# Optimization experiments

Hardware: AMD Instinct MI355X
Metric: run time of the kernel (lower is better)

## Reference

```python
import jax, jax.numpy as jnp
import numpy as np

BN_EPS = 1e-5
TAU = 1.0  # gumbel temperature

def setup_inputs() -> dict:
    key = jax.random.key(0)
    ks = jax.random.split(key, 6)
    B, O, F, H, HID = 32, 4096, 256, 8, 128
    x = jax.random.normal(ks[0], (B, O, F), dtype=jnp.float32)
    gumbel_noise = jax.random.gumbel(ks[1], (B, O, H), dtype=jnp.float32)
    W_in = jax.random.normal(ks[2], (F, HID), dtype=jnp.float32) * (1.0 / np.sqrt(F))
    b_in = jnp.zeros((HID,), jnp.float32)
    W_blk = jax.random.normal(ks[3], (HID, HID), dtype=jnp.float32) * (1.0 / np.sqrt(HID))
    b_blk = jnp.zeros((HID,), jnp.float32)
    bn_gamma = jnp.ones((HID,), jnp.float32)
    bn_beta = jnp.zeros((HID,), jnp.float32)
    W_fc = jax.random.normal(ks[4], (HID, H), dtype=jnp.float32) * (1.0 / np.sqrt(HID))
    b_fc = jnp.zeros((H,), jnp.float32)
    return {"x": x, "gumbel_noise": gumbel_noise, "W_in": W_in, "b_in": b_in,
            "W_blk": W_blk, "b_blk": b_blk, "bn_gamma": bn_gamma, "bn_beta": bn_beta,
            "W_fc": W_fc, "b_fc": b_fc}

def reference(x, gumbel_noise, W_in, b_in, W_blk, b_blk, bn_gamma, bn_beta, W_fc, b_fc):
    B, O, F = x.shape
    xf = x.reshape(B * O, F)
    # DynamicNetwork head: input linear + relu, one residual block (Linear+BN+ReLU), fc
    h = jax.nn.relu(xf @ W_in + b_in)  # (B*O, HID)
    z = h @ W_blk + b_blk
    mu = z.mean(axis=0)
    var = z.var(axis=0)  # biased var, matches BatchNorm training normalization
    z = (z - mu) * jax.lax.rsqrt(var + BN_EPS) * bn_gamma + bn_beta
    h = jax.nn.relu(z) + h  # residual
    logits = (h @ W_fc + b_fc).reshape(B, O, -1)  # (B, O, H)
    # mask out zero-norm observations
    mask = (jnp.linalg.norm(x, axis=2) != 0)[..., None].astype(x.dtype)  # (B, O, 1)
    logits = logits * mask
    # gumbel softmax over observation dim (soft)
    w = jax.nn.softmax((logits + gumbel_noise) / TAU, axis=1)  # (B, O, H)
    # weighted sum pooling: algebraically the repeat-multiply-sum in the original
    pooled = jnp.einsum('boh,bof->bhf', w, x)  # (B, H, F)
    return pooled.reshape(B, -1)  # (B, H*F)
```

## Files before the change

### kernel.cpp

```cpp
#include <hip/hip_runtime.h>
#include <math.h>

#define MB_ 131072
#define F_  256
#define HID_ 128
#define H_  8
#define O_  4096
#define B_  32

typedef __attribute__((ext_vector_type(8))) short short8;
typedef __attribute__((ext_vector_type(4))) float f32x4;

static __device__ __forceinline__ unsigned short f2bf(float f) {
    unsigned int u = __float_as_uint(f);
    unsigned int r = (u + 0x7fffu + ((u >> 16) & 1u)) >> 16;
    return (unsigned short)r;
}
static __device__ __forceinline__ float bflo(unsigned int u) {
    return __uint_as_float(u << 16);
}
static __device__ __forceinline__ float bfhi(unsigned int u) {
    return __uint_as_float(u & 0xffff0000u);
}
static __device__ __forceinline__ unsigned int fkey(float f) {
    unsigned int u = __float_as_uint(f);
    return (u & 0x80000000u) ? ~u : (u | 0x80000000u);
}
static __device__ __forceinline__ short8 pack_bf16x8(const float4 a, const float4 b) {
    short8 r;
    r[0] = (short)f2bf(a.x); r[1] = (short)f2bf(a.y);
    r[2] = (short)f2bf(a.z); r[3] = (short)f2bf(a.w);
    r[4] = (short)f2bf(b.x); r[5] = (short)f2bf(b.y);
    r[6] = (short)f2bf(b.z); r[7] = (short)f2bf(b.w);
    return r;
}
static __device__ __forceinline__ void sync_lds() {
    asm volatile("s_waitcnt lgkmcnt(0)" ::: "memory");
    __builtin_amdgcn_s_barrier();
    __builtin_amdgcn_sched_barrier(0);
}

__global__ __launch_bounds__(256) void k_prep(
    const float* __restrict__ W_in, const float* __restrict__ W_blk,
    unsigned short* __restrict__ WinT, unsigned short* __restrict__ WblkT,
    unsigned int* __restrict__ Mmax)
{
    const int idx = blockIdx.x * 256 + threadIdx.x;
    if (idx < 256) Mmax[idx] = 0u;
    if (idx < 32768) {
        const int n = idx >> 8, k = idx & 255;
        WinT[idx] = f2bf(W_in[(size_t)k * HID_ + n]);
    } else {
        const int i2 = idx - 32768;
        const int n = i2 >> 7, k = i2 & 127;
        WblkT[i2] = f2bf(W_blk[(size_t)k * HID_ + n]);
    }
}

__global__ __launch_bounds__(512, 4) void k_fused(
    const float* __restrict__ x, const unsigned short* __restrict__ WinT,
    const float* __restrict__ b_in,
    const unsigned short* __restrict__ WblkT, const float* __restrict__ b_blk,
    unsigned short* __restrict__ h_out, unsigned short* __restrict__ z_out,
    float* __restrict__ mask_out,
    float* __restrict__ sumP, float* __restrict__ sumsqP)
{
    __shared__ unsigned short smem[16384];
    unsigned short* stg = smem;
    unsigned short* h_s = smem;

    const int tid = threadIdx.x;
    const int R0 = blockIdx.x * 128;
    const int wave = tid >> 6;
    const int wrow = wave >> 2;
    const int wcol = wave & 3;
    const int lane = tid & 63;
    const int lm = lane & 15, quad = lane >> 4;

    const int srow = tid >> 2, sch = tid & 3;
    const int sgo = srow * 32 + ((sch ^ ((srow >> 1) & 3)) << 3);
    const float* xb = x + (size_t)(R0 + srow) * F_ + sch * 8;

    int aoff[4];
#pragma unroll
    for (int mi = 0; mi < 4; mi++) {
        const int ar = wrow * 64 + mi * 16 + lm;
        aoff[mi] = ar * 32 + ((quad ^ ((ar >> 1) & 3)) << 3);
    }
    const unsigned short* wr0 = WinT + (size_t)(wcol * 32 + lm) * F_ + quad * 8;
    const unsigned short* wr1 = wr0 + (size_t)16 * F_;

    f32x4 acc[4][2];
#pragma unroll
    for (int i = 0; i < 4; i++)
#pragma unroll
        for (int j = 0; j < 2; j++) acc[i][j] = (f32x4){0.f, 0.f, 0.f, 0.f};
    float msq = 0.f;

    float4 c0 = *(const float4*)(xb);
    float4 c1 = *(const float4*)(xb + 4);

#pragma unroll
    for (int kt = 0; kt < 8; kt++) {
        float4 n0, n1;
        if (kt < 7) {
            n0 = *(const float4*)(xb + (kt + 1) * 32);
            n1 = *(const float4*)(xb + (kt + 1) * 32 + 4);
        }
        short8 bC[2];
        bC[0] = *(const short8*)(wr0 + kt * 32);
        bC[1] = *(const short8*)(wr1 + kt * 32);
        msq += c0.x * c0.x + c0.y * c0.y + c0.z * c0.z + c0.w * c0.w
             + c1.x * c1.x + c1.y * c1.y + c1.z * c1.z + c1.w * c1.w;
        *(short8*)(stg + (kt & 1) * 4096 + sgo) = pack_bf16x8(c0, c1);
        sync_lds();
        short8 af[4];
#pragma unroll
        for (int mi = 0; mi < 4; mi++)
            af[mi] = *(const short8*)(stg + (kt & 1) * 4096 + aoff[mi]);
#pragma unroll
        for (int mi = 0; mi < 4; mi++)
#pragma unroll
            for (int ni = 0; ni < 2; ni++)
                acc[mi][ni] = __builtin_amdgcn_mfma_f32_16x16x32_bf16(af[mi], bC[ni], acc[mi][ni], 0, 0, 0);
        if (kt < 7) { c0 = n0; c1 = n1; }
    }

    msq += __shfl_xor(msq, 1, 64);
    msq += __shfl_xor(msq, 2, 64);
    if ((tid & 3) == 0) mask_out[R0 + srow] = (msq != 0.f) ? 1.f : 0.f;

    __syncthreads();

    {
        float bcol[2];
#pragma unroll
        for (int ni = 0; ni < 2; ni++) bcol[ni] = b_in[wcol * 32 + ni * 16 + lm];
#pragma unroll
        for (int mi = 0; mi < 4; mi++)
#pragma unroll
            for (int r = 0; r < 4; r++) {
                const int rl = wrow * 64 + mi * 16 + quad * 4 + r;
#pragma unroll
                for (int ni = 0; ni < 2; ni++) {
                    const int col = wcol * 32 + ni * 16 + lm;
                    const float v = fmaxf(acc[mi][ni][r] + bcol[ni], 0.f);
                    h_s[rl * 128 + ((((col >> 3) ^ (rl & 7)) << 3) | (col & 7))] = f2bf(v);
                }
            }
    }
#pragma unroll
    for (int i = 0; i < 4; i++)
#pragma unroll
        for (int j = 0; j < 2; j++) acc[i][j] = (f32x4){0.f, 0.f, 0.f, 0.f};
    __syncthreads();

    {
        const int crow = tid >> 2, cb = tid & 3;
#pragma unroll
        for (int j = 0; j < 4; j++) {
            const int ch = cb * 4 + j;
            const short8 v = *(const short8*)(h_s + crow * 128 + ((ch ^ (crow & 7)) << 3));
            *(short8*)(h_out + (size_t)(R0 + crow) * HID_ + ch * 8) = v;
        }
    }

    {
        const unsigned short* wb0 = WblkT + (size_t)(wcol * 32 + lm) * HID_ + quad * 8;
        const unsigned short* wb1 = wb0 + (size_t)16 * HID_;
#pragma unroll
        for (int kt2 = 0; kt2 < 4; kt2++) {
            short8 wbf[2];
            wbf[0] = *(const short8*)(wb0 + kt2 * 32);
            wbf[1] = *(const short8*)(wb1 + kt2 * 32);
            short8 haf[4];
#pragma unroll
            for (int mi = 0; mi < 4; mi++) {
                const int hr = wrow * 64 + mi * 16 + lm;
                haf[mi] = *(const short8*)(h_s + hr * 128 + (((kt2 * 4 + quad) ^ (hr & 7)) << 3));
            }
#pragma unroll
            for (int mi = 0; mi < 4; mi++)
#pragma unroll
                for (int ni = 0; ni < 2; ni++)
                    acc[mi][ni] = __builtin_amdgcn_mfma_f32_16x16x32_bf16(haf[mi], wbf[ni], acc[mi][ni], 0, 0, 0);
        }
    }

    __syncthreads();

    {
        float bcol2[2];
#pragma unroll
        for (int ni = 0; ni < 2; ni++) bcol2[ni] = b_blk[wcol * 32 + ni * 16 + lm];
        float s_c[2] = {0.f, 0.f}, ss_c[2] = {0.f, 0.f};
#pragma unroll
        for (int mi = 0; mi < 4; mi++)
#pragma unroll
            for (int r = 0; r < 4; r++) {
                const int rl = wrow * 64 + mi * 16 + quad * 4 + r;
#pragma unroll
                for (int ni = 0; ni < 2; ni++) {
                    const int col = wcol * 32 + ni * 16 + lm;
                    const float zv = acc[mi][ni][r] + bcol2[ni];
                    s_c[ni] += zv;
                    ss_c[ni] += zv * zv;
                    h_s[rl * 128 + ((((col >> 3) ^ (rl & 7)) << 3) | (col & 7))] = f2bf(zv);
                }
            }
#pragma unroll
        for (int ni = 0; ni < 2; ni++) {
            s_c[ni]  += __shfl_xor(s_c[ni], 16, 64);
            s_c[ni]  += __shfl_xor(s_c[ni], 32, 64);
            ss_c[ni] += __shfl_xor(ss_c[ni], 16, 64);
            ss_c[ni] += __shfl_xor(ss_c[ni], 32, 64);
        }
        if (quad == 0) {
#pragma unroll
            for (int ni = 0; ni < 2; ni++) {
                const int col = wcol * 32 + ni * 16 + lm;
                sumP[((size_t)blockIdx.x * 2 + wrow) * 128 + col]   = s_c[ni];
                sumsqP[((size_t)blockIdx.x * 2 + wrow) * 128 + col] = ss_c[ni];
            }
        }
    }
    __syncthreads();

    {
        const int crow = tid >> 2, cb = tid & 3;
#pragma unroll
        for (int j = 0; j < 4; j++) {
            const int ch = cb * 4 + j;
            const short8 v = *(const short8*)(h_s + crow * 128 + ((ch ^ (crow & 7)) << 3));
            *(short8*)(z_out + (size_t)(R0 + crow) * HID_ + ch * 8) = v;
        }
    }
}

__global__ __launch_bounds__(256) void k_bnfin(
    const float* __restrict__ sumP, const float* __restrict__ sumsqP,
    const float* __restrict__ gamma, const float* __restrict__ beta,
    float* __restrict__ scale, float* __restrict__ shift)
{
    const int c = blockIdx.x;
    const int tid = threadIdx.x;
    float s = 0.f, ss = 0.f;
    for (int i = tid; i < 2048; i += 256) {
        s  += sumP[(size_t)i * 128 + c];
        ss += sumsqP[(size_t)i * 128 + c];
    }
#pragma unroll
    for (int off = 32; off; off >>= 1) {
        s  += __shfl_xor(s, off, 64);
        ss += __shfl_xor(ss, off, 64);
    }
    __shared__ float rs[4], rss[4];
    const int wid = tid >> 6, lane = tid & 63;
    if (lane == 0) { rs[wid] = s; rss[wid] = ss; }
    __syncthreads();
    if (tid == 0) {
        const float S  = rs[0] + rs[1] + rs[2] + rs[3];
        const float SS = rss[0] + rss[1] + rss[2] + rss[3];
        const float inv_m = 1.0f / (float)MB_;
        const float mu = S * inv_m;
        const float var = SS * inv_m - mu * mu;
        const float sc = gamma[c] * rsqrtf(var + 1e-5f);
        scale[c] = sc;
        shift[c] = beta[c] - mu * sc;
    }
}

__global__ __launch_bounds__(256) void k_logits(
    const unsigned short* __restrict__ h_in, const unsigned short* __restrict__ z_in,
    const float* __restrict__ scale, const float* __restrict__ shift,
    const float* __restrict__ W_fc, const float* __restrict__ b_fc,
    const float* __restrict__ mask, const float* __restrict__ gumbel,
    float* __restrict__ t_out, unsigned int* __restrict__ Mmax)
{
    __shared__ float wfc_s[1024];
    __shared__ float sc_s[128], sh_s[128];
    const int tid = threadIdx.x;
    for (int i = tid; i < 1024; i += 256) wfc_s[i] = W_fc[i];
    if (tid < 128) { sc_s[tid] = scale[tid]; sh_s[tid] = shift[tid]; }
    __syncthreads();

    const size_t row0 = (size_t)blockIdx.x * 512 + tid;
    const size_t row1 = row0 + 256;
    float a0[8], a1[8];
#pragma unroll
    for (int j = 0; j < 8; j++) { a0[j] = 0.f; a1[j] = 0.f; }

    const uint4* hp0 = (const uint4*)(h_in + row0 * HID_);
    const uint4* zq0 = (const uint4*)(z_in + row0 * HID_);
    const uint4* hp1 = (const uint4*)(h_in + row1 * HID_);
    const uint4* zq1 = (const uint4*)(z_in + row1 * HID_);

#pragma unroll 2
    for (int kc = 0; kc < 16; kc++) {
        const uint4 h0 = hp0[kc], z0 = zq0[kc];
        const uint4 h1 = hp1[kc], z1 = zq1[kc];
        const unsigned int hs0[4] = {h0.x, h0.y, h0.z, h0.w};
        const unsigned int zs0[4] = {z0.x, z0.y, z0.z, z0.w};
        const unsigned int hs1[4] = {h1.x, h1.y, h1.z, h1.w};
        const unsigned int zs1[4] = {z1.x, z1.y, z1.z, z1.w};
#pragma unroll
        for (int p = 0; p < 4; p++) {
            const int k = kc * 8 + p * 2;
            const float sck0 = sc_s[k], shk0 = sh_s[k];
            const float sck1 = sc_s[k + 1], shk1 = sh_s[k + 1];
            const float4 wA = *(const float4*)&wfc_s[k * 8];
            const float4 wB = *(const float4*)&wfc_s[k * 8 + 4];
            const float4 wC = *(const float4*)&wfc_s[k * 8 + 8];
            const float4 wD = *(const float4*)&wfc_s[k * 8 + 12];
            {
                const float hf0 = bflo(hs0[p]), hf1 = bfhi(hs0[p]);
                const float zf0 = bflo(zs0[p]), zf1 = bfhi(zs0[p]);
                const float hb0 = fmaxf(zf0 * sck0 + shk0, 0.f) + hf0;
                const float hb1 = fmaxf(zf1 * sck1 + shk1, 0.f) + hf1;
                a0[0] += hb0 * wA.x + hb1 * wC.x;  a0[1] += hb0 * wA.y + hb1 * wC.y;
                a0[2] += hb0 * wA.z + hb1 * wC.z;  a0[3] += hb0 * wA.w + hb1 * wC.w;
                a0[4] += hb0 * wB.x + hb1 * wD.x;  a0[5] += hb0 * wB.y + hb1 * wD.y;
                a0[6] += hb0 * wB.z + hb1 * wD.z;  a0[7] += hb0 * wB.w + hb1 * wD.w;
            }
            {
                const float hf0 = bflo(hs1[p]), hf1 = bfhi(hs1[p]);
                const float zf0 = bflo(zs1[p]), zf1 = bfhi(zs1[p]);
                const float hb0 = fmaxf(zf0 * sck0 + shk0, 0.f) + hf0;
                const float hb1 = fmaxf(zf1 * sck1 + shk1, 0.f) + hf1;
                a1[0] += hb0 * wA.x + hb1 * wC.x;  a1[1] += hb0 * wA.y + hb1 * wC.y;
                a1[2] += hb0 * wA.z + hb1 * wC.z;  a1[3] += hb0 * wA.w + hb1 * wC.w;
                a1[4] += hb0 * wB.x + hb1 * wD.x;  a1[5] += hb0 * wB.y + hb1 * wD.y;
                a1[6] += hb0 * wB.z + hb1 * wD.z;  a1[7] += hb0 * wB.w + hb1 * wD.w;
            }
        }
    }

    float bf[8];
#pragma unroll
    for (int j = 0; j < 8; j++) bf[j] = b_fc[j];
    const float mk0 = mask[row0], mk1 = mask[row1];
    float g0[8], g1[8];
    *(float4*)&g0[0] = *(const float4*)(gumbel + row0 * 8);
    *(float4*)&g0[4] = *(const float4*)(gumbel + row0 * 8 + 4);
    *(float4*)&g1[0] = *(const float4*)(gumbel + row1 * 8);
    *(float4*)&g1[4] = *(const float4*)(gumbel + row1 * 8 + 4);
    float t0[8], t1[8];
#pragma unroll
    for (int j = 0; j < 8; j++) {
        t0[j] = (a0[j] + bf[j]) * mk0 + g0[j];
        t1[j] = (a1[j] + bf[j]) * mk1 + g1[j];
    }
    *(float4*)(t_out + row0 * 8)     = *(float4*)&t0[0];
    *(float4*)(t_out + row0 * 8 + 4) = *(float4*)&t0[4];
    *(float4*)(t_out + row1 * 8)     = *(float4*)&t1[0];
    *(float4*)(t_out + row1 * 8 + 4) = *(float4*)&t1[4];

    float tm[8];
#pragma unroll
    for (int j = 0; j < 8; j++) tm[j] = fmaxf(t0[j], t1[j]);
#pragma unroll
    for (int off = 32; off; off >>= 1)
#pragma unroll
        for (int j = 0; j < 8; j++) tm[j] = fmaxf(tm[j], __shfl_xor(tm[j], off, 64));
    if ((tid & 63) == 0) {
        const int bb = blockIdx.x >> 3;
#pragma unroll
        for (int j = 0; j < 8; j++) atomicMax(&Mmax[bb * 8 + j], fkey(tm[j]));
    }
}

__global__ __launch_bounds__(256) void k_pool(
    const float* __restrict__ x, const float* __restrict__ t_in,
    const unsigned int* __restrict__ Mmax,
    float* __restrict__ pp, float* __restrict__ zp)
{
    __shared__ float ws_s[8][64];
    __shared__ float M_s[8];
    const int tid = threadIdx.x;
    const int oc = blockIdx.x;
    const int b  = blockIdx.y;
    if (tid < 8) {
        const unsigned int k = Mmax[b * 8 + tid];
        const unsigned int s = (k & 0x80000000u) ? (k & 0x7fffffffu) : ~k;
        M_s[tid] = __uint_as_float(s);
    }
    __syncthreads();
#pragma unroll
    for (int i = tid; i < 512; i += 256) {
        const int ol = i >> 3, hh = i & 7;
        const float tv = t_in[((size_t)b * O_ + oc * 64 + ol) * H_ + hh];
        ws_s[hh][ol] = __expf(tv - M_s[hh]);
    }
    __syncthreads();
    if (tid < 8) {
        float s = 0.f;
        for (int o = 0; o < 64; o++) s += ws_s[tid][o];
        zp[((size_t)oc * 32 + b) * 8 + tid] = s;
    }
    float acc[8];
#pragma unroll
    for (int hh = 0; hh < 8; hh++) acc[hh] = 0.f;
    const float* xp = x + ((size_t)b * O_ + oc * 64) * F_ + tid;
#pragma unroll 4
    for (int o = 0; o < 64; o++) {
        const float xv = xp[(size_t)o * F_];
#pragma unroll
        for (int hh = 0; hh < 8; hh++) acc[hh] += ws_s[hh][o] * xv;
    }
    float* outp = pp + ((size_t)oc * 32 + b) * 2048;
#pragma unroll
    for (int hh = 0; hh < 8; hh++) outp[hh * 256 + tid] = acc[hh];
}

__global__ __launch_bounds__(256) void k_reduce(
    const float* __restrict__ pp, const float* __restrict__ zp,
    float* __restrict__ out)
{
    const int blk = blockIdx.x;
    const int b = blk >> 3, hh = blk & 7;
    const int tid = threadIdx.x;
    __shared__ float invZ_s;
    if (tid < 64) {
        float z = zp[((size_t)tid * 32 + b) * 8 + hh];
#pragma unroll
        for (int off = 32; off; off >>= 1) z += __shfl_xor(z, off, 64);
        if (tid == 0) invZ_s = 1.f / z;
    }
    __syncthreads();
    float s = 0.f;
    const float* p0 = pp + (size_t)b * 2048 + hh * 256 + tid;
#pragma unroll 8
    for (int ocq = 0; ocq < 64; ocq++) s += p0[(size_t)ocq * 65536];
    out[(size_t)b * 2048 + hh * 256 + tid] = s * invZ_s;
}

extern "C" void kernel_launch(void* const* d_in, const int* in_sizes, int n_in,
                              void* d_out, int out_size, void* d_ws, size_t ws_size,
                              hipStream_t stream)
{
    const float* x      = (const float*)d_in[0];
    const float* gumbel = (const float*)d_in[1];
    const float* W_in   = (const float*)d_in[2];
    const float* b_in   = (const float*)d_in[3];
    const float* W_blk  = (const float*)d_in[4];
    const float* b_blk  = (const float*)d_in[5];
    const float* gamma  = (const float*)d_in[6];
    const float* beta   = (const float*)d_in[7];
    const float* W_fc   = (const float*)d_in[8];
    const float* b_fc   = (const float*)d_in[9];
    float* out = (float*)d_out;
    char* ws = (char*)d_ws;

    unsigned short* h_bf  = (unsigned short*)(ws + 0);
    float* pp     = (float*)(ws + 0);
    float* zp     = (float*)(ws + 16777216);
    unsigned short* z_bf  = (unsigned short*)(ws + 33554432);
    float* mask   = (float*)(ws + 67108864);
    float* sumP   = (float*)(ws + 67633152);
    float* sumsqP = (float*)(ws + 68681728);
    float* scale  = (float*)(ws + 69730304);
    float* shift  = (float*)(ws + 69730816);
    float* t_buf  = (float*)(ws + 69731328);
    unsigned int* Mmax = (unsigned int*)(ws + 73925632);
    unsigned short* WinT  = (unsigned short*)(ws + 73926656);
    unsigned short* WblkT = (unsigned short*)(ws + 73992192);

    k_prep<<<192, 256, 0, stream>>>(W_in, W_blk, WinT, WblkT, Mmax);
    k_fused<<<1024, 512, 0, stream>>>(x, WinT, b_in, WblkT, b_blk, h_bf, z_bf, mask, sumP, sumsqP);
    k_bnfin<<<128, 256, 0, stream>>>(sumP, sumsqP, gamma, beta, scale, shift);
    k_logits<<<256, 256, 0, stream>>>(h_bf, z_bf, scale, shift, W_fc, b_fc, mask, gumbel, t_buf, Mmax);
    k_pool<<<dim3(64, 32), 256, 0, stream>>>(x, t_buf, Mmax, pp, zp);
    k_reduce<<<256, 256, 0, stream>>>(pp, zp, out);
}
```

Measured before the change: 303.9 us.

## Stage x tiles via global_load_lds and convert to bf16 after the LDS read

Replaces the register-staged x loads (global load, pack to bf16, LDS store) with direct global-to-LDS DMA loads of fp32 data into a double-buffered, XOR-swizzled LDS tile. Each wave then reads fp32 from LDS, computes the row squared-norm for the mask, and packs to bf16 before the MFMA. The aim is to cut VGPR pressure and VALU/store work on the load path and overlap the prefetch with compute. In exchange, LDS traffic doubles because fp32 is stored, the bf16 conversion is repeated by all four wcol waves, and each k-step now waits on vmcnt(0) plus a barrier.

Result: slower. 311.0 us (+2.4%).

```diff
diff --git a/kernel.cpp b/kernel.cpp
--- a/kernel.cpp
+++ b/kernel.cpp
@@ -34,10 +34,10 @@
     r[6] = (short)f2bf(b.z); r[7] = (short)f2bf(b.w);
     return r;
 }
-static __device__ __forceinline__ void sync_lds() {
-    asm volatile("s_waitcnt lgkmcnt(0)" ::: "memory");
-    __builtin_amdgcn_s_barrier();
-    __builtin_amdgcn_sched_barrier(0);
+static __device__ __forceinline__ void gll16(const float* g, float* l) {
+    __builtin_amdgcn_global_load_lds(
+        (const __attribute__((address_space(1))) float*)g,
+        (__attribute__((address_space(3))) float*)l, 16, 0, 0);
 }
 
 __global__ __launch_bounds__(256) void k_prep(
@@ -66,7 +66,7 @@
     float* __restrict__ sumP, float* __restrict__ sumsqP)
 {
     __shared__ unsigned short smem[16384];
-    unsigned short* stg = smem;
+    float* stgf = (float*)smem;
     unsigned short* h_s = smem;
 
     const int tid = threadIdx.x;
@@ -77,15 +77,20 @@
     const int lane = tid & 63;
     const int lm = lane & 15, quad = lane >> 4;
 
-    const int srow = tid >> 2, sch = tid & 3;
-    const int sgo = srow * 32 + ((sch ^ ((srow >> 1) & 3)) << 3);
-    const float* xb = x + (size_t)(R0 + srow) * F_ + sch * 8;
-
-    int aoff[4];
+    const int r0s = wave * 16 + (lane >> 3);
+    const int r1s = r0s + 8;
+    const int cl0 = (lane & 7) ^ (r0s & 7);
+    const int cl1 = (lane & 7) ^ (r1s & 7);
+    const float* g0 = x + (size_t)(R0 + r0s) * F_ + cl0 * 4;
+    const float* g1 = x + (size_t)(R0 + r1s) * F_ + cl1 * 4;
+    const int lbase = wave * 512;
+
+    int aoff[4][2];
 #pragma unroll
     for (int mi = 0; mi < 4; mi++) {
         const int ar = wrow * 64 + mi * 16 + lm;
-        aoff[mi] = ar * 32 + ((quad ^ ((ar >> 1) & 3)) << 3);
+        aoff[mi][0] = ar * 32 + (((2 * quad) ^ (ar & 7)) << 2);
+        aoff[mi][1] = ar * 32 + (((2 * quad + 1) ^ (ar & 7)) << 2);
     }
     const unsigned short* wr0 = WinT + (size_t)(wcol * 32 + lm) * F_ + quad * 8;
     const unsigned short* wr1 = wr0 + (size_t)16 * F_;
@@ -95,41 +100,54 @@
     for (int i = 0; i < 4; i++)
 #pragma unroll
         for (int j = 0; j < 2; j++) acc[i][j] = (f32x4){0.f, 0.f, 0.f, 0.f};
-    float msq = 0.f;
-
-    float4 c0 = *(const float4*)(xb);
-    float4 c1 = *(const float4*)(xb + 4);
+    float msq[4] = {0.f, 0.f, 0.f, 0.f};
+
+    gll16(g0, stgf + lbase);
+    gll16(g1, stgf + lbase + 256);
+    asm volatile("s_waitcnt vmcnt(0)" ::: "memory");
+    __builtin_amdgcn_s_barrier();
+    __builtin_amdgcn_sched_barrier(0);
 
 #pragma unroll
     for (int kt = 0; kt < 8; kt++) {
-        float4 n0, n1;
+        const int b = kt & 1;
+        const short8 bC0 = *(const short8*)(wr0 + kt * 32);
+        const short8 bC1 = *(const short8*)(wr1 + kt * 32);
         if (kt < 7) {
-            n0 = *(const float4*)(xb + (kt + 1) * 32);
-            n1 = *(const float4*)(xb + (kt + 1) * 32 + 4);
-        }
-        short8 bC[2];
-        bC[0] = *(const short8*)(wr0 + kt * 32);
-        bC[1] = *(const short8*)(wr1 + kt * 32);
-        msq += c0.x * c0.x + c0.y * c0.y + c0.z * c0.z + c0.w * c0.w
-             + c1.x * c1.x + c1.y * c1.y + c1.z * c1.z + c1.w * c1.w;
-        *(short8*)(stg + (kt & 1) * 4096 + sgo) = pack_bf16x8(c0, c1);
-        sync_lds();
+            float* d = stgf + (b ^ 1) * 4096 + lbase;
+            gll16(g0 + (kt + 1) * 32, d);
+            gll16(g1 + (kt + 1) * 32, d + 256);
+        }
         short8 af[4];
 #pragma unroll
-        for (int mi = 0; mi < 4; mi++)
-            af[mi] = *(const short8*)(stg + (kt & 1) * 4096 + aoff[mi]);
-#pragma unroll
-        for (int mi = 0; mi < 4; mi++)
-#pragma unroll
-            for (int ni = 0; ni < 2; ni++)
-                acc[mi][ni] = __builtin_amdgcn_mfma_f32_16x16x32_bf16(af[mi], bC[ni], acc[mi][ni], 0, 0, 0);
-        if (kt < 7) { c0 = n0; c1 = n1; }
-    }
-
-    msq += __shfl_xor(msq, 1, 64);
-    msq += __shfl_xor(msq, 2, 64);
-    if ((tid & 3) == 0) mask_out[R0 + srow] = (msq != 0.f) ? 1.f : 0.f;
-
+        for (int mi = 0; mi < 4; mi++) {
+            const float4 fa = *(const float4*)(stgf + b * 4096 + aoff[mi][0]);
+            const float4 fb = *(const float4*)(stgf + b * 4096 + aoff[mi][1]);
+            if (wcol == 0)
+                msq[mi] += fa.x * fa.x + fa.y * fa.y + fa.z * fa.z + fa.w * fa.w
+                         + fb.x * fb.x + fb.y * fb.y + fb.z * fb.z + fb.w * fb.w;
+            af[mi] = pack_bf16x8(fa, fb);
+        }
+#pragma unroll
+        for (int mi = 0; mi < 4; mi++) {
+            acc[mi][0] = __builtin_amdgcn_mfma_f32_16x16x32_bf16(af[mi], bC0, acc[mi][0], 0, 0, 0);
+            acc[mi][1] = __builtin_amdgcn_mfma_f32_16x16x32_bf16(af[mi], bC1, acc[mi][1], 0, 0, 0);
+        }
+        asm volatile("s_waitcnt vmcnt(0)" ::: "memory");
+        __builtin_amdgcn_s_barrier();
+        __builtin_amdgcn_sched_barrier(0);
+    }
+
+    if (wcol == 0) {
+#pragma unroll
+        for (int mi = 0; mi < 4; mi++) {
+            float m = msq[mi];
+            m += __shfl_xor(m, 16, 64);
+            m += __shfl_xor(m, 32, 64);
+            if (quad == 0)
+                mask_out[R0 + wrow * 64 + mi * 16 + lm] = (m != 0.f) ? 1.f : 0.f;
+        }
+    }
     __syncthreads();
 
     {
```

## Fold residual h@W_fc into fused kernel, drop h round-trip to memory

Applied to the files above, without the earlier changes.

The residual term h@W_fc is split out by linearity and computed inside the fused GEMM kernel from the shared-memory h tile, so only an 8-float-per-row partial is written instead of the full bf16 h matrix. The logits kernel then reads just z plus the small partial, which removes about 32 MB of write and read traffic. The logits kernel is also relaunched with one row per thread across twice as many blocks. The trade-off is extra scalar FMA work and LDS reads in the fused kernel, plus slightly more shared memory that could affect occupancy.

New measurement: 306.4 us. Within noise of the previous version (+0.8%).

```diff
diff --git a/kernel.cpp b/kernel.cpp
--- a/kernel.cpp
+++ b/kernel.cpp
@@ -15,6 +15,9 @@
     unsigned int u = __float_as_uint(f);
     unsigned int r = (u + 0x7fffu + ((u >> 16) & 1u)) >> 16;
     return (unsigned short)r;
+}
+static __device__ __forceinline__ float bf2f(unsigned short u) {
+    return __uint_as_float(((unsigned int)u) << 16);
 }
 static __device__ __forceinline__ float bflo(unsigned int u) {
     return __uint_as_float(u << 16);
@@ -61,13 +64,15 @@
     const float* __restrict__ x, const unsigned short* __restrict__ WinT,
     const float* __restrict__ b_in,
     const unsigned short* __restrict__ WblkT, const float* __restrict__ b_blk,
-    unsigned short* __restrict__ h_out, unsigned short* __restrict__ z_out,
+    const float* __restrict__ W_fc,
+    unsigned short* __restrict__ z_out, float* __restrict__ hw,
     float* __restrict__ mask_out,
     float* __restrict__ sumP, float* __restrict__ sumsqP)
 {
-    __shared__ unsigned short smem[16384];
+    __shared__ unsigned short smem[18432];
     unsigned short* stg = smem;
     unsigned short* h_s = smem;
+    float* wfc_ls = (float*)(smem + 16384);
 
     const int tid = threadIdx.x;
     const int R0 = blockIdx.x * 128;
@@ -76,6 +81,9 @@
     const int wcol = wave & 3;
     const int lane = tid & 63;
     const int lm = lane & 15, quad = lane >> 4;
+
+    wfc_ls[tid] = W_fc[tid];
+    wfc_ls[tid + 512] = W_fc[tid + 512];
 
     const int srow = tid >> 2, sch = tid & 3;
     const int sgo = srow * 32 + ((sch ^ ((srow >> 1) & 3)) << 3);
@@ -156,13 +164,22 @@
     __syncthreads();
 
     {
-        const int crow = tid >> 2, cb = tid & 3;
-#pragma unroll
-        for (int j = 0; j < 4; j++) {
-            const int ch = cb * 4 + j;
-            const short8 v = *(const short8*)(h_s + crow * 128 + ((ch ^ (crow & 7)) << 3));
-            *(short8*)(h_out + (size_t)(R0 + crow) * HID_ + ch * 8) = v;
-        }
+        const int rw = tid >> 2;
+        const int jp = tid & 3;
+        float a0 = 0.f, a1 = 0.f;
+#pragma unroll
+        for (int c = 0; c < 16; c++) {
+            const short8 hv = *(const short8*)(h_s + rw * 128 + ((c ^ (rw & 7)) << 3));
+#pragma unroll
+            for (int e = 0; e < 8; e++) {
+                const float hf = bf2f((unsigned short)hv[e]);
+                const float2 w = *(const float2*)(wfc_ls + (c * 8 + e) * 8 + 2 * jp);
+                a0 += hf * w.x;
+                a1 += hf * w.y;
+            }
+        }
+        float2 o; o.x = a0; o.y = a1;
+        *(float2*)(hw + ((size_t)(R0 + rw)) * 8 + 2 * jp) = o;
     }
 
     {
@@ -271,7 +288,7 @@
 }
 
 __global__ __launch_bounds__(256) void k_logits(
-    const unsigned short* __restrict__ h_in, const unsigned short* __restrict__ z_in,
+    const unsigned short* __restrict__ z_in, const float* __restrict__ hw,
     const float* __restrict__ scale, const float* __restrict__ shift,
     const float* __restrict__ W_fc, const float* __restrict__ b_fc,
     const float* __restrict__ mask, const float* __restrict__ gumbel,
@@ -284,86 +301,59 @@
     if (tid < 128) { sc_s[tid] = scale[tid]; sh_s[tid] = shift[tid]; }
     __syncthreads();
 
-    const size_t row0 = (size_t)blockIdx.x * 512 + tid;
-    const size_t row1 = row0 + 256;
-    float a0[8], a1[8];
-#pragma unroll
-    for (int j = 0; j < 8; j++) { a0[j] = 0.f; a1[j] = 0.f; }
-
-    const uint4* hp0 = (const uint4*)(h_in + row0 * HID_);
-    const uint4* zq0 = (const uint4*)(z_in + row0 * HID_);
-    const uint4* hp1 = (const uint4*)(h_in + row1 * HID_);
-    const uint4* zq1 = (const uint4*)(z_in + row1 * HID_);
-
-#pragma unroll 2
+    const size_t row = (size_t)blockIdx.x * 256 + tid;
+    float a[8];
+#pragma unroll
+    for (int j = 0; j < 8; j++) a[j] = 0.f;
+
+    const uint4* zq = (const uint4*)(z_in + row * HID_);
+#pragma unroll 4
     for (int kc = 0; kc < 16; kc++) {
-        const uint4 h0 = hp0[kc], z0 = zq0[kc];
-        const uint4 h1 = hp1[kc], z1 = zq1[kc];
-        const unsigned int hs0[4] = {h0.x, h0.y, h0.z, h0.w};
-        const unsigned int zs0[4] = {z0.x, z0.y, z0.z, z0.w};
-        const unsigned int hs1[4] = {h1.x, h1.y, h1.z, h1.w};
-        const unsigned int zs1[4] = {z1.x, z1.y, z1.z, z1.w};
+        const uint4 z0 = zq[kc];
+        const unsigned int zs[4] = {z0.x, z0.y, z0.z, z0.w};
 #pragma unroll
         for (int p = 0; p < 4; p++) {
             const int k = kc * 8 + p * 2;
-            const float sck0 = sc_s[k], shk0 = sh_s[k];
-            const float sck1 = sc_s[k + 1], shk1 = sh_s[k + 1];
+            const float zf0 = bflo(zs[p]), zf1 = bfhi(zs[p]);
+            const float hb0 = fmaxf(zf0 * sc_s[k] + sh_s[k], 0.f);
+            const float hb1 = fmaxf(zf1 * sc_s[k + 1] + sh_s[k + 1], 0.f);
             const float4 wA = *(const float4*)&wfc_s[k * 8];
             const float4 wB = *(const float4*)&wfc_s[k * 8 + 4];
             const float4 wC = *(const float4*)&wfc_s[k * 8 + 8];
             const float4 wD = *(const float4*)&wfc_s[k * 8 + 12];
-            {
-                const float hf0 = bflo(hs0[p]), hf1 = bfhi(hs0[p]);
-                const float zf0 = bflo(zs0[p]), zf1 = bfhi(zs0[p]);
-                const float hb0 = fmaxf(zf0 * sck0 + shk0, 0.f) + hf0;
-                const float hb1 = fmaxf(zf1 * sck1 + shk1, 0.f) + hf1;
-                a0[0] += hb0 * wA.x + hb1 * wC.x;  a0[1] += hb0 * wA.y + hb1 * wC.y;
-                a0[2] += hb0 * wA.z + hb1 * wC.z;  a0[3] += hb0 * wA.w + hb1 * wC.w;
-                a0[4] += hb0 * wB.x + hb1 * wD.x;  a0[5] += hb0 * wB.y + hb1 * wD.y;
-                a0[6] += hb0 * wB.z + hb1 * wD.z;  a0[7] += hb0 * wB.w + hb1 * wD.w;
-            }
-            {
-                const float hf0 = bflo(hs1[p]), hf1 = bfhi(hs1[p]);
-                const float zf0 = bflo(zs1[p]), zf1 = bfhi(zs1[p]);
-                const float hb0 = fmaxf(zf0 * sck0 + shk0, 0.f) + hf0;
-                const float hb1 = fmaxf(zf1 * sck1 + shk1, 0.f) + hf1;
-                a1[0] += hb0 * wA.x + hb1 * wC.x;  a1[1] += hb0 * wA.y + hb1 * wC.y;
-                a1[2] += hb0 * wA.z + hb1 * wC.z;  a1[3] += hb0 * wA.w + hb1 * wC.w;
-                a1[4] += hb0 * wB.x + hb1 * wD.x;  a1[5] += hb0 * wB.y + hb1 * wD.y;
-                a1[6] += hb0 * wB.z + hb1 * wD.z;  a1[7] += hb0 * wB.w + hb1 * wD.w;
-            }
-        }
-    }
-
+            a[0] += hb0 * wA.x + hb1 * wC.x;  a[1] += hb0 * wA.y + hb1 * wC.y;
+            a[2] += hb0 * wA.z + hb1 * wC.z;  a[3] += hb0 * wA.w + hb1 * wC.w;
+            a[4] += hb0 * wB.x + hb1 * wD.x;  a[5] += hb0 * wB.y + hb1 * wD.y;
+            a[6] += hb0 * wB.z + hb1 * wD.z;  a[7] += hb0 * wB.w + hb1 * wD.w;
+        }
+    }
+
+    float hwv[8];
+    *(float4*)&hwv[0] = *(const float4*)(hw + row * 8);
+    *(float4*)&hwv[4] = *(const float4*)(hw + row * 8 + 4);
     float bf[8];
 #pragma unroll
     for (int j = 0; j < 8; j++) bf[j] = b_fc[j];
-    const float mk0 = mask[row0], mk1 = mask[row1];
-    float g0[8], g1[8];
-    *(float4*)&g0[0] = *(const float4*)(gumbel + row0 * 8);
-    *(float4*)&g0[4] = *(const float4*)(gumbel + row0 * 8 + 4);
-    *(float4*)&g1[0] = *(const float4*)(gumbel + row1 * 8);
-    *(float4*)&g1[4] = *(const float4*)(gumbel + row1 * 8 + 4);
-    float t0[8], t1[8];
-#pragma unroll
-    for (int j = 0; j < 8; j++) {
-        t0[j] = (a0[j] + bf[j]) * mk0 + g0[j];
-        t1[j] = (a1[j] + bf[j]) * mk1 + g1[j];
-    }
-    *(float4*)(t_out + row0 * 8)     = *(float4*)&t0[0];
-    *(float4*)(t_out + row0 * 8 + 4) = *(float4*)&t0[4];
-    *(float4*)(t_out + row1 * 8)     = *(float4*)&t1[0];
-    *(float4*)(t_out + row1 * 8 + 4) = *(float4*)&t1[4];
+    const float mk = mask[row];
+    float g[8];
+    *(float4*)&g[0] = *(const float4*)(gumbel + row * 8);
+    *(float4*)&g[4] = *(const float4*)(gumbel + row * 8 + 4);
+    float t[8];
+#pragma unroll
+    for (int j = 0; j < 8; j++)
+        t[j] = (a[j] + hwv[j] + bf[j]) * mk + g[j];
+    *(float4*)(t_out + row * 8)     = *(float4*)&t[0];
+    *(float4*)(t_out + row * 8 + 4) = *(float4*)&t[4];
 
     float tm[8];
 #pragma unroll
-    for (int j = 0; j < 8; j++) tm[j] = fmaxf(t0[j], t1[j]);
+    for (int j = 0; j < 8; j++) tm[j] = t[j];
 #pragma unroll
     for (int off = 32; off; off >>= 1)
 #pragma unroll
         for (int j = 0; j < 8; j++) tm[j] = fmaxf(tm[j], __shfl_xor(tm[j], off, 64));
     if ((tid & 63) == 0) {
-        const int bb = blockIdx.x >> 3;
+        const int bb = blockIdx.x >> 4;
 #pragma unroll
         for (int j = 0; j < 8; j++) atomicMax(&Mmax[bb * 8 + j], fkey(tm[j]));
     }
@@ -451,9 +441,9 @@
     float* out = (float*)d_out;
     char* ws = (char*)d_ws;
 
-    unsigned short* h_bf  = (unsigned short*)(ws + 0);
     float* pp     = (float*)(ws + 0);
     float* zp     = (float*)(ws + 16777216);
+    float* hw     = (float*)(ws + 16842752);
     unsigned short* z_bf  = (unsigned short*)(ws + 33554432);
     float* mask   = (float*)(ws + 67108864);
     float* sumP   = (float*)(ws + 67633152);
@@ -466,9 +456,9 @@
     unsigned short* WblkT = (unsigned short*)(ws + 73992192);
 
     k_prep<<<192, 256, 0, stream>>>(W_in, W_blk, WinT, WblkT, Mmax);
-    k_fused<<<1024, 512, 0, stream>>>(x, WinT, b_in, WblkT, b_blk, h_bf, z_bf, mask, sumP, sumsqP);
+    k_fused<<<1024, 512, 0, stream>>>(x, WinT, b_in, WblkT, b_blk, W_fc, z_bf, hw, mask, sumP, sumsqP);
     k_bnfin<<<128, 256, 0, stream>>>(sumP, sumsqP, gamma, beta, scale, shift);
-    k_logits<<<256, 256, 0, stream>>>(h_bf, z_bf, scale, shift, W_fc, b_fc, mask, gumbel, t_buf, Mmax);
+    k_logits<<<512, 256, 0, stream>>>(z_bf, hw, scale, shift, W_fc, b_fc, mask, gumbel, t_buf, Mmax);
     k_pool<<<dim3(64, 32), 256, 0, stream>>>(x, t_buf, Mmax, pp, zp);
     k_reduce<<<256, 256, 0, stream>>>(pp, zp, out);
 }
```
